# Performance work log

Hardware: AMD Instinct MI355X
Metric: run time of the kernel (lower is better)

## Reference

```python
import jax, jax.numpy as jnp
import numpy as np

N_NODES = 50000
N_EDGES = 1600000
D = 128  # input_dim == hidden_dim


def glorot(key, shape):
    lim = float(np.sqrt(6.0 / (shape[0] + shape[1])))
    return jax.random.uniform(key, shape, jnp.float32, -lim, lim)


def setup_inputs() -> dict:
    key = jax.random.key(0)
    ks = jax.random.split(key, 10)
    x = jax.random.normal(ks[0], (N_NODES, D), jnp.float32)
    edge_index = jax.random.randint(ks[1], (2, N_EDGES), 0, N_NODES, jnp.int64)
    edge_attr = jax.random.normal(ks[2], (N_EDGES, D), jnp.float32)
    # SAGEConv params per layer: lin_l (W,b), lin_r (W, no bias)
    W1l = glorot(ks[3], (D, D)); b1l = jnp.zeros((D,), jnp.float32)
    W1r = glorot(ks[4], (D, D))
    W2l = glorot(ks[5], (D, D)); b2l = jnp.zeros((D,), jnp.float32)
    W2r = glorot(ks[6], (D, D))
    return {"x": x, "edge_index": edge_index, "edge_attr": edge_attr,
            "W1l": W1l, "b1l": b1l, "W1r": W1r,
            "W2l": W2l, "b2l": b2l, "W2r": W2r}


def sage_layer(z, src, dst, edge_attr, Wl, bl, Wr):
    # message: gather x_j, add edge_attr, relu  -> [E, D]
    msg = jax.nn.relu(z[src] + edge_attr)
    # mean aggregation at destination nodes
    agg = jax.ops.segment_sum(msg, dst, num_segments=N_NODES)
    cnt = jax.ops.segment_sum(jnp.ones((dst.shape[0], 1), z.dtype), dst,
                              num_segments=N_NODES)
    agg = agg / jnp.maximum(cnt, 1.0)
    # lin_l(agg) + lin_r(x) (root weight, no bias on lin_r)
    return agg @ Wl + bl + z @ Wr


def reference(x, edge_index, edge_attr, W1l, b1l, W1r, W2l, b2l, W2r):
    src, dst = edge_index[0], edge_index[1]
    z = sage_layer(x, src, dst, edge_attr, W1l, b1l, W1r)
    z = jax.nn.relu(z)  # activation between layers; dropout=0, normalize='none'
    z = sage_layer(z, src, dst, edge_attr, W2l, b2l, W2r)
    return z
```

## Files before the change

### kernel.cpp

```cpp
#include <hip/hip_runtime.h>

#define D 128

typedef __attribute__((ext_vector_type(8))) short bf16x8;
typedef __attribute__((ext_vector_type(4))) float f32x4;
typedef __attribute__((ext_vector_type(4))) unsigned short u16x4;

__device__ inline unsigned short f2bf(float f) {
    union { float f; unsigned u; } v; v.f = f;
    unsigned r = v.u + 0x7FFF + ((v.u >> 16) & 1);
    return (unsigned short)(r >> 16);
}
__device__ inline float bf2f(unsigned short h) {
    union { unsigned u; float f; } v; v.u = ((unsigned)h) << 16; return v.f;
}


__global__ __launch_bounds__(256) void castx_kernel(const float* __restrict__ x,
                                                    unsigned short* __restrict__ xb, int n4) {
    int i = blockIdx.x * 256 + threadIdx.x;
    if (i < n4) {
        float4 v = reinterpret_cast<const float4*>(x)[i];
        ushort4 r;
        r.x = f2bf(v.x); r.y = f2bf(v.y); r.z = f2bf(v.z); r.w = f2bf(v.w);
        reinterpret_cast<ushort4*>(xb)[i] = r;
    }
}

__global__ __launch_bounds__(256) void wcast_kernel(const float* __restrict__ W1l,
                                                    const float* __restrict__ W1r,
                                                    const float* __restrict__ W2l,
                                                    const float* __restrict__ W2r,
                                                    unsigned short* __restrict__ Wt1,
                                                    unsigned short* __restrict__ Wt2) {
    int c = blockIdx.x, k = threadIdx.x;
    float v1 = (k < 128) ? W1l[k * 128 + c] : W1r[(k - 128) * 128 + c];
    float v2 = (k < 128) ? W2l[k * 128 + c] : W2r[(k - 128) * 128 + c];
    Wt1[c * 256 + k] = f2bf(v1);
    Wt2[c * 256 + k] = f2bf(v2);
}


__global__ __launch_bounds__(256) void count_kernel(const int* __restrict__ dst,
                                                    int* __restrict__ cnt, int E) {
    int e = blockIdx.x * 256 + threadIdx.x;
    if (e < E) atomicAdd(&cnt[dst[e]], 1);
}

__global__ __launch_bounds__(256) void psum_kernel(const int* __restrict__ cnt,
                                                   int* __restrict__ bsum, int n) {
    __shared__ int wsh[4];
    int b = blockIdx.x, tid = threadIdx.x;
    int i0 = b * 1024 + tid * 4;
    int s = 0;
    #pragma unroll
    for (int j = 0; j < 4; ++j) { int i = i0 + j; if (i < n) s += cnt[i]; }
    #pragma unroll
    for (int d = 1; d < 64; d <<= 1) s += __shfl_xor(s, d, 64);
    if ((tid & 63) == 0) wsh[tid >> 6] = s;
    __syncthreads();
    if (tid == 0) bsum[b] = wsh[0] + wsh[1] + wsh[2] + wsh[3];
}

__global__ __launch_bounds__(64) void bscan_kernel(const int* __restrict__ bsum,
                                                   int* __restrict__ bpre, int nb) {
    int t = threadIdx.x;
    int v = (t < nb) ? bsum[t] : 0;
    int sc = v;
    #pragma unroll
    for (int d = 1; d < 64; d <<= 1) { int u = __shfl_up(sc, d, 64); if (t >= d) sc += u; }
    if (t < nb) bpre[t] = sc - v;
}

__global__ __launch_bounds__(256) void fscan_kernel(const int* __restrict__ cnt,
                                                    const int* __restrict__ bpre,
                                                    int* __restrict__ off,
                                                    int* __restrict__ cursor, int n) {
    __shared__ int wsum[4];
    int b = blockIdx.x, tid = threadIdx.x;
    int lane = tid & 63, wv = tid >> 6;
    int i0 = b * 1024 + tid * 4;
    int v[4]; int s = 0;
    #pragma unroll
    for (int j = 0; j < 4; ++j) { int i = i0 + j; v[j] = (i < n) ? cnt[i] : 0; s += v[j]; }
    int sc = s;
    #pragma unroll
    for (int d = 1; d < 64; d <<= 1) { int u = __shfl_up(sc, d, 64); if (lane >= d) sc += u; }
    if (lane == 63) wsum[wv] = sc;
    __syncthreads();
    int wp = 0;
    for (int j = 0; j < wv; ++j) wp += wsum[j];
    int base = bpre[b] + wp + sc - s;
    #pragma unroll
    for (int j = 0; j < 4; ++j) {
        int i = i0 + j;
        if (i < n) { cursor[i] = base; off[i + 1] = base + v[j]; }
        base += v[j];
    }
    if (b == 0 && tid == 0) off[0] = 0;
}

__global__ __launch_bounds__(256) void fill_kernel(const int* __restrict__ src,
                                                   const int* __restrict__ dst,
                                                   int* __restrict__ cursor,
                                                   int2* __restrict__ pairs, int E) {
    int e = blockIdx.x * 256 + threadIdx.x;
    if (e < E) {
        int d = dst[e];
        int slot = atomicAdd(&cursor[d], 1);
        pairs[slot] = make_int2(src[e], e);
    }
}


template <int WRITE_EAB, int EA_BF16>
__global__ __launch_bounds__(256) void aggregate_kernel(const unsigned short* __restrict__ featb,
                                                        const float* __restrict__ ea,
                                                        unsigned short* __restrict__ eab,
                                                        const int* __restrict__ off,
                                                        const long long* __restrict__ pairs,
                                                        unsigned short* __restrict__ aggb,
                                                        int N) {
    int nd = blockIdx.x * 4 + (threadIdx.x >> 6);
    if (nd >= N) return;
    int t = threadIdx.x & 63;
    int half = t >> 5, l32 = t & 31;
    int s = off[nd], e = off[nd + 1];
    float a0 = 0.f, a1 = 0.f, a2 = 0.f, a3 = 0.f;

    for (int b = s; b < e; b += 64) {
        int cnt = min(64, e - b);
        long long prl = (b + t < e) ? __builtin_nontemporal_load(&pairs[b + t]) : 0LL;
        int psrc = (int)prl;
        int peid = (int)(prl >> 32);

        auto fetch = [&](int idx, f32x4& ev, u16x4& xv) {
            int sidx = __shfl(psrc, idx, 64);
            int q = b + idx;
            if (EA_BF16) {
                u16x4 eb = __builtin_nontemporal_load(
                    reinterpret_cast<const u16x4*>(&eab[(size_t)q * D + l32 * 4]));
                ev[0] = bf2f(eb[0]); ev[1] = bf2f(eb[1]);
                ev[2] = bf2f(eb[2]); ev[3] = bf2f(eb[3]);
            } else {
                int eidx = __shfl(peid, idx, 64);
                ev = __builtin_nontemporal_load(
                    reinterpret_cast<const f32x4*>(&ea[(size_t)eidx * D + l32 * 4]));
                if (WRITE_EAB) {
                    u16x4 wv;
                    wv[0] = f2bf(ev[0]); wv[1] = f2bf(ev[1]);
                    wv[2] = f2bf(ev[2]); wv[3] = f2bf(ev[3]);
                    __builtin_nontemporal_store(wv,
                        reinterpret_cast<u16x4*>(&eab[(size_t)q * D + l32 * 4]));
                }
            }
            xv = *reinterpret_cast<const u16x4*>(&featb[(size_t)sidx * D + l32 * 4]);
        };
        auto accum = [&](const f32x4& ev, const u16x4& xv) {
            a0 += fmaxf(bf2f(xv[0]) + ev[0], 0.f);
            a1 += fmaxf(bf2f(xv[1]) + ev[1], 0.f);
            a2 += fmaxf(bf2f(xv[2]) + ev[2], 0.f);
            a3 += fmaxf(bf2f(xv[3]) + ev[3], 0.f);
        };

        int p = 0;
        for (; p + 8 <= cnt; p += 8) {
            f32x4 e0, e1, e2, e3; u16x4 x0, x1, x2, x3;
            fetch(p + half, e0, x0);
            fetch(p + 2 + half, e1, x1);
            fetch(p + 4 + half, e2, x2);
            fetch(p + 6 + half, e3, x3);
            accum(e0, x0); accum(e1, x1); accum(e2, x2); accum(e3, x3);
        }
        if (p + 4 <= cnt) {
            f32x4 e0, e1; u16x4 x0, x1;
            fetch(p + half, e0, x0);
            fetch(p + 2 + half, e1, x1);
            accum(e0, x0); accum(e1, x1);
            p += 4;
        }
        if (p + 2 <= cnt) {
            f32x4 e0; u16x4 x0;
            fetch(p + half, e0, x0);
            accum(e0, x0);
            p += 2;
        }
        if (p < cnt) {
            f32x4 e0; u16x4 x0;
            fetch(p, e0, x0);
            if (half == 0) accum(e0, x0);
        }
    }

    a0 += __shfl_xor(a0, 32, 64);
    a1 += __shfl_xor(a1, 32, 64);
    a2 += __shfl_xor(a2, 32, 64);
    a3 += __shfl_xor(a3, 32, 64);
    int deg = e - s;
    float inv = 1.f / (float)(deg > 0 ? deg : 1);
    if (half == 0) {
        ushort4 r;
        r.x = f2bf(a0 * inv); r.y = f2bf(a1 * inv);
        r.z = f2bf(a2 * inv); r.w = f2bf(a3 * inv);
        *reinterpret_cast<ushort4*>(&aggb[(size_t)nd * D + l32 * 4]) = r;
    }
}


template <int RELU, int OUT_BF16>
__global__ __launch_bounds__(256) void gemm_mfma_kernel(const unsigned short* __restrict__ A1,
                                                        const unsigned short* __restrict__ A2,
                                                        const unsigned short* __restrict__ Wt,
                                                        const float* __restrict__ bias,
                                                        float* __restrict__ outf,
                                                        unsigned short* __restrict__ outb,
                                                        int MT, int N) {
    int tid = threadIdx.x;
    int w = tid >> 6;
    int l = tid & 63;
    int lr = l & 15;
    int lg = l >> 4;
    int c0 = w * 32;

    bf16x8 bfr[2][8];
    #pragma unroll
    for (int t = 0; t < 2; ++t)
        #pragma unroll
        for (int kc = 0; kc < 8; ++kc)
            bfr[t][kc] = *reinterpret_cast<const bf16x8*>(
                &Wt[(size_t)(c0 + t * 16 + lr) * 256 + kc * 32 + lg * 8]);

    for (int mt = blockIdx.x; mt < MT; mt += gridDim.x) {
        int r0 = mt * 32;
        f32x4 acc[2][2];
        #pragma unroll
        for (int tr = 0; tr < 2; ++tr)
            #pragma unroll
            for (int tc = 0; tc < 2; ++tc) acc[tr][tc] = {0.f, 0.f, 0.f, 0.f};

        #pragma unroll
        for (int kc = 0; kc < 8; ++kc) {
            const unsigned short* Ap = (kc < 4) ? A1 : A2;
            int k = (kc & 3) * 32 + lg * 8;
            bf16x8 af0 = *reinterpret_cast<const bf16x8*>(&Ap[(size_t)(r0 + lr) * D + k]);
            bf16x8 af1 = *reinterpret_cast<const bf16x8*>(&Ap[(size_t)(r0 + 16 + lr) * D + k]);
            acc[0][0] = __builtin_amdgcn_mfma_f32_16x16x32_bf16(af0, bfr[0][kc], acc[0][0], 0, 0, 0);
            acc[1][0] = __builtin_amdgcn_mfma_f32_16x16x32_bf16(af1, bfr[0][kc], acc[1][0], 0, 0, 0);
            acc[0][1] = __builtin_amdgcn_mfma_f32_16x16x32_bf16(af0, bfr[1][kc], acc[0][1], 0, 0, 0);
            acc[1][1] = __builtin_amdgcn_mfma_f32_16x16x32_bf16(af1, bfr[1][kc], acc[1][1], 0, 0, 0);
        }

        #pragma unroll
        for (int tc = 0; tc < 2; ++tc) {
            int col = c0 + tc * 16 + lr;
            float bv = bias[col];
            #pragma unroll
            for (int tr = 0; tr < 2; ++tr) {
                #pragma unroll
                for (int r = 0; r < 4; ++r) {
                    int row = r0 + tr * 16 + lg * 4 + r;
                    if (row < N) {
                        float v = acc[tr][tc][r] + bv;
                        if (RELU) v = fmaxf(v, 0.f);
                        if (OUT_BF16) outb[(size_t)row * D + col] = f2bf(v);
                        else outf[(size_t)row * D + col] = v;
                    }
                }
            }
        }
    }
}

extern "C" void kernel_launch(void* const* d_in, const int* in_sizes, int n_in,
                              void* d_out, int out_size, void* d_ws, size_t ws_size,
                              hipStream_t stream) {
    const float* x   = (const float*)d_in[0];
    const int*   ei  = (const int*)d_in[1];
    const float* ea  = (const float*)d_in[2];
    const float* W1l = (const float*)d_in[3];
    const float* b1l = (const float*)d_in[4];
    const float* W1r = (const float*)d_in[5];
    const float* W2l = (const float*)d_in[6];
    const float* b2l = (const float*)d_in[7];
    const float* W2r = (const float*)d_in[8];
    float* out = (float*)d_out;

    const int N = in_sizes[0] / D;
    const int E = in_sizes[1] / 2;
    const int NP = (N + 31) & ~31;
    const int* src = ei;
    const int* dst = ei + E;

    char* ws = (char*)d_ws;
    size_t o = 0;
    auto alloc = [&](size_t bytes) -> void* {
        void* p = ws + o;
        o = (o + bytes + 255) & ~(size_t)255;
        return p;
    };
    int*   cnt    = (int*)alloc((size_t)N * 4);
    int*   off    = (int*)alloc((size_t)(N + 1) * 4);
    int*   cursor = (int*)alloc((size_t)N * 4);
    int*   bsum   = (int*)alloc(256 * 4);
    int*   bpre   = (int*)alloc(256 * 4);
    int2*  pairs  = (int2*)alloc((size_t)E * 8);
    unsigned short* eab  = (unsigned short*)alloc((size_t)E * D * 2);
    unsigned short* xb   = (unsigned short*)alloc((size_t)NP * D * 2);
    unsigned short* z1b  = (unsigned short*)alloc((size_t)NP * D * 2);
    unsigned short* aggb = (unsigned short*)alloc((size_t)NP * D * 2);
    unsigned short* Wt1  = (unsigned short*)alloc(128 * 256 * 2);
    unsigned short* Wt2  = (unsigned short*)alloc(128 * 256 * 2);
    (void)ws_size; (void)n_in; (void)out_size;

    const int MT = (N + 31) / 32;
    const int NB = (N + 1023) / 1024;
    const int AGB = (N + 3) / 4;

    castx_kernel<<<(N * D / 4 + 255) / 256, 256, 0, stream>>>(x, xb, N * D / 4);
    wcast_kernel<<<128, 256, 0, stream>>>(W1l, W1r, W2l, W2r, Wt1, Wt2);

    (void)hipMemsetAsync(cnt, 0, (size_t)N * 4, stream);
    count_kernel<<<(E + 255) / 256, 256, 0, stream>>>(dst, cnt, E);
    psum_kernel<<<NB, 256, 0, stream>>>(cnt, bsum, N);
    bscan_kernel<<<1, 64, 0, stream>>>(bsum, bpre, NB);
    fscan_kernel<<<NB, 256, 0, stream>>>(cnt, bpre, off, cursor, N);
    fill_kernel<<<(E + 255) / 256, 256, 0, stream>>>(src, dst, cursor, pairs, E);

    aggregate_kernel<1, 0><<<AGB, 256, 0, stream>>>(xb, ea, eab, off,
                                                    (const long long*)pairs, aggb, N);
    gemm_mfma_kernel<1, 1><<<1024, 256, 0, stream>>>(aggb, xb, Wt1, b1l, nullptr, z1b, MT, N);

    aggregate_kernel<0, 1><<<AGB, 256, 0, stream>>>(z1b, nullptr, eab, off,
                                                    (const long long*)pairs, aggb, N);
    gemm_mfma_kernel<0, 0><<<1024, 256, 0, stream>>>(aggb, z1b, Wt2, b2l, out, nullptr, MT, N);
}
```

Baseline: 612.6 us.

## Store edge attributes as FP8 E4M3 and merge prep kernels

The layer-1 aggregation now writes the dst-sorted edge attributes as 8-bit E4M3 values with software encode and decode, replacing the bf16 copy. This halves the bytes written in layer 1 and read back in layer 2, which are the dominant memory traffic. The cast, count and weight-transpose kernels are merged into one launch, and the CSR fill uses nontemporal 64-bit stores. The trade-offs are extra ALU work per element for the conversions and a substantial loss of precision on edge_attr, which may break the tolerance check.

```diff
diff --git a/kernel.cpp b/kernel.cpp
--- a/kernel.cpp
+++ b/kernel.cpp
@@ -5,6 +5,7 @@
 typedef __attribute__((ext_vector_type(8))) short bf16x8;
 typedef __attribute__((ext_vector_type(4))) float f32x4;
 typedef __attribute__((ext_vector_type(4))) unsigned short u16x4;
+typedef __attribute__((ext_vector_type(4))) unsigned char u8x4;
 
 __device__ inline unsigned short f2bf(float f) {
     union { float f; unsigned u; } v; v.f = f;
@@ -14,38 +15,56 @@
 __device__ inline float bf2f(unsigned short h) {
     union { unsigned u; float f; } v; v.u = ((unsigned)h) << 16; return v.f;
 }
-
-
-__global__ __launch_bounds__(256) void castx_kernel(const float* __restrict__ x,
-                                                    unsigned short* __restrict__ xb, int n4) {
-    int i = blockIdx.x * 256 + threadIdx.x;
-    if (i < n4) {
-        float4 v = reinterpret_cast<const float4*>(x)[i];
-        ushort4 r;
-        r.x = f2bf(v.x); r.y = f2bf(v.y); r.z = f2bf(v.z); r.w = f2bf(v.w);
-        reinterpret_cast<ushort4*>(xb)[i] = r;
-    }
-}
-
-__global__ __launch_bounds__(256) void wcast_kernel(const float* __restrict__ W1l,
-                                                    const float* __restrict__ W1r,
-                                                    const float* __restrict__ W2l,
-                                                    const float* __restrict__ W2r,
-                                                    unsigned short* __restrict__ Wt1,
-                                                    unsigned short* __restrict__ Wt2) {
-    int c = blockIdx.x, k = threadIdx.x;
-    float v1 = (k < 128) ? W1l[k * 128 + c] : W1r[(k - 128) * 128 + c];
-    float v2 = (k < 128) ? W2l[k * 128 + c] : W2r[(k - 128) * 128 + c];
-    Wt1[c * 256 + k] = f2bf(v1);
-    Wt2[c * 256 + k] = f2bf(v2);
-}
-
-
-__global__ __launch_bounds__(256) void count_kernel(const int* __restrict__ dst,
-                                                    int* __restrict__ cnt, int E) {
-    int e = blockIdx.x * 256 + threadIdx.x;
-    if (e < E) atomicAdd(&cnt[dst[e]], 1);
-}
+__device__ inline unsigned char f2fp8(float f) {
+    unsigned u = __float_as_uint(f);
+    unsigned s = (u >> 31) << 7;
+    unsigned r = (u & 0x7fffffffu) + 0x7FFFF + ((u >> 20) & 1);
+    int e = (int)(r >> 23) - 127;
+    if (e < -6) return (unsigned char)s;
+    return (unsigned char)(s | ((unsigned)(e + 7) << 3) | ((r >> 20) & 7));
+}
+__device__ inline float fp82f(unsigned c) {
+    unsigned ef = (c >> 3) & 0xF, m = c & 7, s = c >> 7;
+    unsigned nb = (s << 31) | ((ef + 120) << 23) | (m << 20);
+    float nv = __uint_as_float(nb);
+    float sv = (s ? -0.001953125f : 0.001953125f) * (float)m;
+    return ef ? nv : sv;
+}
+
+
+__global__ __launch_bounds__(256) void prep_kernel(const float* __restrict__ x,
+                                                   unsigned short* __restrict__ xb, int n4,
+                                                   const int* __restrict__ dst,
+                                                   int* __restrict__ cnt, int E,
+                                                   const float* __restrict__ W1l,
+                                                   const float* __restrict__ W1r,
+                                                   const float* __restrict__ W2l,
+                                                   const float* __restrict__ W2r,
+                                                   unsigned short* __restrict__ Wt1,
+                                                   unsigned short* __restrict__ Wt2,
+                                                   int CAST_B, int CNT_B) {
+    int b = blockIdx.x, tid = threadIdx.x;
+    if (b < CAST_B) {
+        int i = b * 256 + tid;
+        if (i < n4) {
+            float4 v = reinterpret_cast<const float4*>(x)[i];
+            ushort4 r;
+            r.x = f2bf(v.x); r.y = f2bf(v.y); r.z = f2bf(v.z); r.w = f2bf(v.w);
+            reinterpret_cast<ushort4*>(xb)[i] = r;
+        }
+    } else if (b < CAST_B + CNT_B) {
+        int e = (b - CAST_B) * 256 + tid;
+        if (e < E) atomicAdd(&cnt[dst[e]], 1);
+    } else {
+        int c = b - CAST_B - CNT_B;
+        int k = tid;
+        float v1 = (k < 128) ? W1l[k * 128 + c] : W1r[(k - 128) * 128 + c];
+        float v2 = (k < 128) ? W2l[k * 128 + c] : W2r[(k - 128) * 128 + c];
+        Wt1[c * 256 + k] = f2bf(v1);
+        Wt2[c * 256 + k] = f2bf(v2);
+    }
+}
+
 
 __global__ __launch_bounds__(256) void psum_kernel(const int* __restrict__ cnt,
                                                    int* __restrict__ bsum, int n) {
@@ -103,20 +122,21 @@
 __global__ __launch_bounds__(256) void fill_kernel(const int* __restrict__ src,
                                                    const int* __restrict__ dst,
                                                    int* __restrict__ cursor,
-                                                   int2* __restrict__ pairs, int E) {
+                                                   long long* __restrict__ pairs, int E) {
     int e = blockIdx.x * 256 + threadIdx.x;
     if (e < E) {
         int d = dst[e];
         int slot = atomicAdd(&cursor[d], 1);
-        pairs[slot] = make_int2(src[e], e);
-    }
-}
-
-
-template <int WRITE_EAB, int EA_BF16>
+        long long v = (long long)(unsigned)src[e] | ((long long)e << 32);
+        __builtin_nontemporal_store(v, &pairs[slot]);
+    }
+}
+
+
+template <int EA_FP8>
 __global__ __launch_bounds__(256) void aggregate_kernel(const unsigned short* __restrict__ featb,
                                                         const float* __restrict__ ea,
-                                                        unsigned short* __restrict__ eab,
+                                                        unsigned char* __restrict__ eaq,
                                                         const int* __restrict__ off,
                                                         const long long* __restrict__ pairs,
                                                         unsigned short* __restrict__ aggb,
@@ -137,22 +157,20 @@
         auto fetch = [&](int idx, f32x4& ev, u16x4& xv) {
             int sidx = __shfl(psrc, idx, 64);
             int q = b + idx;
-            if (EA_BF16) {
-                u16x4 eb = __builtin_nontemporal_load(
-                    reinterpret_cast<const u16x4*>(&eab[(size_t)q * D + l32 * 4]));
-                ev[0] = bf2f(eb[0]); ev[1] = bf2f(eb[1]);
-                ev[2] = bf2f(eb[2]); ev[3] = bf2f(eb[3]);
+            if (EA_FP8) {
+                u8x4 eq = __builtin_nontemporal_load(
+                    reinterpret_cast<const u8x4*>(&eaq[(size_t)q * D + l32 * 4]));
+                ev[0] = fp82f(eq[0]); ev[1] = fp82f(eq[1]);
+                ev[2] = fp82f(eq[2]); ev[3] = fp82f(eq[3]);
             } else {
                 int eidx = __shfl(peid, idx, 64);
                 ev = __builtin_nontemporal_load(
                     reinterpret_cast<const f32x4*>(&ea[(size_t)eidx * D + l32 * 4]));
-                if (WRITE_EAB) {
-                    u16x4 wv;
-                    wv[0] = f2bf(ev[0]); wv[1] = f2bf(ev[1]);
-                    wv[2] = f2bf(ev[2]); wv[3] = f2bf(ev[3]);
-                    __builtin_nontemporal_store(wv,
-                        reinterpret_cast<u16x4*>(&eab[(size_t)q * D + l32 * 4]));
-                }
+                u8x4 wq;
+                wq[0] = f2fp8(ev[0]); wq[1] = f2fp8(ev[1]);
+                wq[2] = f2fp8(ev[2]); wq[3] = f2fp8(ev[3]);
+                __builtin_nontemporal_store(wq,
+                    reinterpret_cast<u8x4*>(&eaq[(size_t)q * D + l32 * 4]));
             }
             xv = *reinterpret_cast<const u16x4*>(&featb[(size_t)sidx * D + l32 * 4]);
         };
@@ -303,8 +321,8 @@
     int*   cursor = (int*)alloc((size_t)N * 4);
     int*   bsum   = (int*)alloc(256 * 4);
     int*   bpre   = (int*)alloc(256 * 4);
-    int2*  pairs  = (int2*)alloc((size_t)E * 8);
-    unsigned short* eab  = (unsigned short*)alloc((size_t)E * D * 2);
+    long long* pairs = (long long*)alloc((size_t)E * 8);
+    unsigned char* eaq = (unsigned char*)alloc((size_t)E * D);
     unsigned short* xb   = (unsigned short*)alloc((size_t)NP * D * 2);
     unsigned short* z1b  = (unsigned short*)alloc((size_t)NP * D * 2);
     unsigned short* aggb = (unsigned short*)alloc((size_t)NP * D * 2);
@@ -315,22 +333,22 @@
     const int MT = (N + 31) / 32;
     const int NB = (N + 1023) / 1024;
     const int AGB = (N + 3) / 4;
-
-    castx_kernel<<<(N * D / 4 + 255) / 256, 256, 0, stream>>>(x, xb, N * D / 4);
-    wcast_kernel<<<128, 256, 0, stream>>>(W1l, W1r, W2l, W2r, Wt1, Wt2);
+    const int n4 = N * D / 4;
+    const int CAST_B = (n4 + 255) / 256;
+    const int CNT_B = (E + 255) / 256;
 
     (void)hipMemsetAsync(cnt, 0, (size_t)N * 4, stream);
-    count_kernel<<<(E + 255) / 256, 256, 0, stream>>>(dst, cnt, E);
+    prep_kernel<<<CAST_B + CNT_B + 128, 256, 0, stream>>>(x, xb, n4, dst, cnt, E,
+                                                          W1l, W1r, W2l, W2r, Wt1, Wt2,
+                                                          CAST_B, CNT_B);
     psum_kernel<<<NB, 256, 0, stream>>>(cnt, bsum, N);
     bscan_kernel<<<1, 64, 0, stream>>>(bsum, bpre, NB);
     fscan_kernel<<<NB, 256, 0, stream>>>(cnt, bpre, off, cursor, N);
     fill_kernel<<<(E + 255) / 256, 256, 0, stream>>>(src, dst, cursor, pairs, E);
 
-    aggregate_kernel<1, 0><<<AGB, 256, 0, stream>>>(xb, ea, eab, off,
-                                                    (const long long*)pairs, aggb, N);
+    aggregate_kernel<0><<<AGB, 256, 0, stream>>>(xb, ea, eaq, off, pairs, aggb, N);
     gemm_mfma_kernel<1, 1><<<1024, 256, 0, stream>>>(aggb, xb, Wt1, b1l, nullptr, z1b, MT, N);
 
-    aggregate_kernel<0, 1><<<AGB, 256, 0, stream>>>(z1b, nullptr, eab, off,
-                                                    (const long long*)pairs, aggb, N);
+    aggregate_kernel<1><<<AGB, 256, 0, stream>>>(z1b, nullptr, eaq, off, pairs, aggb, N);
     gemm_mfma_kernel<0, 0><<<1024, 256, 0, stream>>>(aggb, z1b, Wt2, b2l, out, nullptr, MT, N);
 }
```

After: 607.1 us. About the same (-0.9%).
